# Kernel tuning notes

Hardware: AMD Instinct MI355X
Metric: run time of the kernel (lower is better)

The kernel has to match this reference:

```python
import jax, jax.numpy as jnp
import numpy as np

N = 10000          # nodes
E = 320000         # edges (~32 neighbors/node)
HID = 128          # hidden_channels
NF = 128           # num_filters
NG = 50            # num_gaussians
NB = 6             # num_interactions
CUT = 10.0         # cutoff


def ssp(x):
    # ShiftedSoftplus: softplus(x) - log(2)
    return jax.nn.softplus(x) - jnp.log(2.0).astype(x.dtype)


def setup_inputs() -> dict:
    key = jax.random.key(0)
    ks = jax.random.split(key, 16)
    z = jax.random.randint(ks[0], (N,), 0, 100)
    pos = jax.random.uniform(ks[1], (N, 3), dtype=jnp.float32) * 5.0  # box so d < cutoff
    row = jax.random.randint(ks[2], (E,), 0, N)
    off = jax.random.randint(ks[3], (E,), 1, N)  # avoid self-loops (radius_graph excludes them)
    col = (row + off) % N
    edge_index = jnp.stack([row, col], axis=0)
    nrm = lambda k, s: 0.1 * jax.random.normal(k, s, dtype=jnp.float32)
    return {
        "z": z,
        "pos": pos,
        "edge_index": edge_index,
        "emb": nrm(ks[4], (100, HID)),
        "mlp_w1": nrm(ks[5], (NB, NG, NF)),
        "mlp_b1": jnp.zeros((NB, NF), jnp.float32),
        "mlp_w2": nrm(ks[6], (NB, NF, NF)),
        "mlp_b2": jnp.zeros((NB, NF), jnp.float32),
        "cl1_w": nrm(ks[7], (NB, HID, NF)),
        "cl2_w": nrm(ks[8], (NB, NF, HID)),
        "cl2_b": jnp.zeros((NB, HID), jnp.float32),
        "lin_w": nrm(ks[9], (NB, HID, HID)),
        "lin_b": jnp.zeros((NB, HID), jnp.float32),
        "out_w1": nrm(ks[10], (HID, HID // 2)),
        "out_b1": jnp.zeros((HID // 2,), jnp.float32),
        "out_w2": nrm(ks[11], (HID // 2, 1)),
        "out_b2": jnp.zeros((1,), jnp.float32),
    }


def schnet_fwd(z, pos, edge_index, emb, mlp_w1, mlp_b1, mlp_w2, mlp_b2,
               cl1_w, cl2_w, cl2_b, lin_w, lin_b, out_w1, out_b1, out_w2, out_b2):
    row, col = edge_index[0], edge_index[1]  # j (source), i (target)
    d = jnp.linalg.norm(pos[row] - pos[col], axis=-1)  # [E]
    offsets = jnp.linspace(0.0, CUT, NG)
    coeff = -0.5 / (offsets[1] - offsets[0]) ** 2
    edge_attr = jnp.exp(coeff * (d[:, None] - offsets) ** 2)  # [E, NG]
    C = 0.5 * (jnp.cos(d * jnp.pi / CUT) + 1.0)  # cosine cutoff [E]
    h = emb[z]  # [N, HID]
    n = h.shape[0]
    for k in range(NB):
        # per-edge filter MLP
        W = ssp(edge_attr @ mlp_w1[k] + mlp_b1[k]) @ mlp_w2[k] + mlp_b2[k]
        W = W * C[:, None]  # [E, NF]
        x = h @ cl1_w[k]  # lin1 (no bias) [N, NF]
        msg = x[row] * W  # gather + modulate
        agg = jax.ops.segment_sum(msg, col, num_segments=n)  # scatter-add to targets
        x = agg @ cl2_w[k] + cl2_b[k]  # lin2 [N, HID]
        x = ssp(x)
        x = x @ lin_w[k] + lin_b[k]  # InteractionBlock.lin
        h = h + x  # residual
    h = ssp(h @ out_w1 + out_b1)
    return h @ out_w2 + out_b2  # [N, 1]


def reference(z, pos, edge_index, emb, mlp_w1, mlp_b1, mlp_w2, mlp_b2,
              cl1_w, cl2_w, cl2_b, lin_w, lin_b, out_w1, out_b1, out_w2, out_b2):
    return schnet_fwd(z, pos, edge_index, emb, mlp_w1, mlp_b1, mlp_w2, mlp_b2,
                      cl1_w, cl2_w, cl2_b, lin_w, lin_b, out_w1, out_b1, out_w2, out_b2)
```

## Files before the change

### kernel.cpp

```cpp
#include <hip/hip_runtime.h>
#include <math.h>

#define N_NODES 10000
#define N_EDGES 320000
#define HID 128
#define NF 128
#define NG 50
#define NB 6
#define SCAN_CH 40
#define WFRAG_PER_K 24576
#define NWF_PER_MAT 32768
#define TBL_M 2048
#define DMAX 8.6602540378f

typedef __attribute__((ext_vector_type(8))) short bf16x8;
typedef __attribute__((ext_vector_type(4))) float f32x4;
typedef __attribute__((ext_vector_type(4))) unsigned int u32x4;

__device__ __forceinline__ int pi_map(int f) {
  return (f & ~31) | ((f & 15) << 1) | ((f >> 4) & 1);
}
__device__ __forceinline__ int pinv_map(int g) {
  return (g & ~31) | ((g & 1) << 4) | ((g & 31) >> 1);
}

__device__ __forceinline__ unsigned short f2bf(float f) {
  unsigned u = __float_as_uint(f);
  u += 0x7FFFu + ((u >> 16) & 1u);
  return (unsigned short)(u >> 16);
}
__device__ __forceinline__ float bf2f(unsigned short s) {
  return __uint_as_float(((unsigned)s) << 16);
}
__device__ __forceinline__ unsigned pack2f(float a, float b) {
  return ((__float_as_uint(a) + 0x8000u) >> 16) |
         ((__float_as_uint(b) + 0x8000u) & 0xFFFF0000u);
}
__device__ __forceinline__ float ssp_fast(float x) {
  float t = __expf(-fabsf(x));
  return fmaxf(x, 0.0f) + __logf(1.0f + t) - 0.69314718055994530942f;
}

__global__ __launch_bounds__(256) void k_embed(const int* __restrict__ z,
                                               const float* __restrict__ emb,
                                               float* __restrict__ h) {
  int t = blockIdx.x * 256 + threadIdx.x;
  if (t >= N_NODES * HID) return;
  int i = t >> 7, c = t & 127;
  h[t] = emb[z[i] * HID + c];
}

__global__ __launch_bounds__(256) void k_hist(const int* __restrict__ col,
                                              int* __restrict__ count) {
  int e = blockIdx.x * 256 + threadIdx.x;
  if (e < N_EDGES) atomicAdd(&count[col[e]], 1);
}

__global__ __launch_bounds__(256) void k_scan(const int* __restrict__ count,
                                              int* __restrict__ rowptr,
                                              int* __restrict__ cursor) {
  __shared__ int s_part[256];
  int t = threadIdx.x;
  int begin = t * SCAN_CH, end = min(begin + SCAN_CH, N_NODES);
  int s = 0;
  for (int i = begin; i < end; i++) s += count[i];
  s_part[t] = s;
  __syncthreads();
  for (int off = 1; off < 256; off <<= 1) {
    int v = (t >= off) ? s_part[t - off] : 0;
    __syncthreads();
    s_part[t] += v;
    __syncthreads();
  }
  int run = (t > 0) ? s_part[t - 1] : 0;
  for (int i = begin; i < end; i++) {
    rowptr[i] = run;
    cursor[i] = run;
    run += count[i];
  }
  if (t == 255) rowptr[N_NODES] = N_EDGES;
}

__global__ __launch_bounds__(256) void k_scatter(const int* __restrict__ row,
                                                 const int* __restrict__ col,
                                                 const float* __restrict__ pos,
                                                 int* __restrict__ cursor,
                                                 int2* __restrict__ sorted_ru) {
  int e = blockIdx.x * 256 + threadIdx.x;
  if (e >= N_EDGES) return;
  int c = col[e], r = row[e];
  float dx = pos[3 * r + 0] - pos[3 * c + 0];
  float dy = pos[3 * r + 1] - pos[3 * c + 1];
  float dz = pos[3 * r + 2] - pos[3 * c + 2];
  float d = sqrtf(dx * dx + dy * dy + dz * dz);
  int p = atomicAdd(&cursor[c], 1);
  float u = d * ((float)(TBL_M - 1) / DMAX);
  sorted_ru[p] = make_int2(r, __float_as_int(u));
}

__global__ __launch_bounds__(256) void k_pack(const float* __restrict__ w1,
                                              const float* __restrict__ w2,
                                              unsigned short* __restrict__ wf) {
  const float* w1k = w1 + (size_t)blockIdx.x * NG * NF;
  const float* w2k = w2 + (size_t)blockIdx.x * NF * NF;
  unsigned short* wfk = wf + (size_t)blockIdx.x * WFRAG_PER_K;
  for (int inst = threadIdx.x; inst < 3072; inst += 256) {
    int fi = inst >> 8;
    int wv = (inst >> 6) & 3;
    int lane = inst & 63;
    int r16 = lane & 15, kgrp = lane >> 4;
    bf16x8 v;
#pragma unroll
    for (int j = 0; j < 8; ++j) {
      float val;
      if (fi < 4) {
        int ncol = wv * 32 + r16 + (fi >> 1) * 16;
        int k = (fi & 1) * 32 + kgrp * 8 + j;
        val = (k < NG) ? w1k[k * NF + ncol] : 0.f;
      } else {
        int fi2 = fi - 4;
        int ncol = wv * 32 + r16 + (fi2 >> 2) * 16;
        int kpi = (fi2 & 3) * 32 + kgrp * 8 + j;
        val = w2k[pinv_map(kpi) * NF + ncol];
      }
      v[j] = (short)f2bf(val);
    }
    *(bf16x8*)&wfk[inst * 8] = v;
  }
}

__global__ __launch_bounds__(256) void k_packn(const float* __restrict__ cl1,
                                               const float* __restrict__ cl2,
                                               const float* __restrict__ lin,
                                               unsigned short* __restrict__ nwf) {
  const int mat = blockIdx.x;
  const float* src = (mat < 6) ? cl1 + (size_t)mat * HID * NF
                   : (mat < 12) ? cl2 + (size_t)(mat - 6) * NF * HID
                                : lin + (size_t)(mat - 12) * HID * HID;
  unsigned short* dst = nwf + (size_t)mat * NWF_PER_MAT;
  for (int inst = threadIdx.x; inst < 2048; inst += 256) {
    int fi = inst >> 8;
    int wv = (inst >> 6) & 3;
    int lane = inst & 63;
    int r16 = lane & 15, kgrp = lane >> 4;
    int ncol = wv * 32 + r16 + (fi >> 2) * 16;
    int kb = fi & 3;
    bf16x8 fh, fl;
#pragma unroll
    for (int j = 0; j < 8; ++j) {
      float val = src[(kb * 32 + kgrp * 8 + j) * 128 + ncol];
      unsigned short hh = f2bf(val);
      fh[j] = (short)hh;
      fl[j] = (short)f2bf(val - bf2f(hh));
    }
    *(bf16x8*)&dst[((fi * 4 + wv) * 64 + lane) * 8] = fh;
    *(bf16x8*)&dst[(((fi + 8) * 4 + wv) * 64 + lane) * 8] = fl;
  }
}

__device__ __forceinline__ void stage_hilo(unsigned short* s_hi, unsigned short* s_lo,
                                           int rr, int c4, float4 v) {
  int cs = c4 ^ ((rr & 7) << 3);
  unsigned hax = (__float_as_uint(v.x) + 0x8000u) & 0xFFFF0000u;
  unsigned hay = (__float_as_uint(v.y) + 0x8000u) & 0xFFFF0000u;
  unsigned haz = (__float_as_uint(v.z) + 0x8000u) & 0xFFFF0000u;
  unsigned haw = (__float_as_uint(v.w) + 0x8000u) & 0xFFFF0000u;
  float lx = v.x - __uint_as_float(hax);
  float ly = v.y - __uint_as_float(hay);
  float lz = v.z - __uint_as_float(haz);
  float lw = v.w - __uint_as_float(haw);
  *(uint2*)&s_hi[rr * 128 + cs] = make_uint2((hax >> 16) | hay, (haz >> 16) | haw);
  *(uint2*)&s_lo[rr * 128 + cs] = make_uint2(pack2f(lx, ly), pack2f(lz, lw));
}

__device__ __forceinline__ int swz_idx(int row, int col) {
  return row * 128 + (((col & ~7) ^ ((row & 7) << 3)) | (col & 7));
}

#define KSTEP(accA, accB, kb, BH_A, BL_A, BH_B, BL_B)                          \
  {                                                                            \
    bf16x8 ahi = *(const bf16x8*)&s_hi[r16 * 128 + (((kb) * 32 + kb0) ^ swz)]; \
    bf16x8 alo = *(const bf16x8*)&s_lo[r16 * 128 + (((kb) * 32 + kb0) ^ swz)]; \
    accA = __builtin_amdgcn_mfma_f32_16x16x32_bf16(ahi, BH_A, accA, 0, 0, 0);  \
    accA = __builtin_amdgcn_mfma_f32_16x16x32_bf16(alo, BH_A, accA, 0, 0, 0);  \
    accA = __builtin_amdgcn_mfma_f32_16x16x32_bf16(ahi, BL_A, accA, 0, 0, 0);  \
    accB = __builtin_amdgcn_mfma_f32_16x16x32_bf16(ahi, BH_B, accB, 0, 0, 0);  \
    accB = __builtin_amdgcn_mfma_f32_16x16x32_bf16(alo, BH_B, accB, 0, 0, 0);  \
    accB = __builtin_amdgcn_mfma_f32_16x16x32_bf16(ahi, BL_B, accB, 0, 0, 0);  \
  }
#define MFMA_HALF(A0, A1)                          \
  {                                                \
    KSTEP(A0, A1, 0, bh00, bl00, bh10, bl10);      \
    KSTEP(A0, A1, 1, bh01, bl01, bh11, bl11);      \
    KSTEP(A0, A1, 2, bh02, bl02, bh12, bl12);      \
    KSTEP(A0, A1, 3, bh03, bl03, bh13, bl13);      \
  }
#define LOAD_FRAGS(wfp)                                                              \
  const bf16x8* np = (const bf16x8*)(wfp);                                           \
  const bf16x8 bh00 = np[(0 * 4 + wvid) * 64 + lane], bh01 = np[(1 * 4 + wvid) * 64 + lane], \
               bh02 = np[(2 * 4 + wvid) * 64 + lane], bh03 = np[(3 * 4 + wvid) * 64 + lane], \
               bh10 = np[(4 * 4 + wvid) * 64 + lane], bh11 = np[(5 * 4 + wvid) * 64 + lane], \
               bh12 = np[(6 * 4 + wvid) * 64 + lane], bh13 = np[(7 * 4 + wvid) * 64 + lane], \
               bl00 = np[(8 * 4 + wvid) * 64 + lane], bl01 = np[(9 * 4 + wvid) * 64 + lane], \
               bl02 = np[(10 * 4 + wvid) * 64 + lane], bl03 = np[(11 * 4 + wvid) * 64 + lane], \
               bl10 = np[(12 * 4 + wvid) * 64 + lane], bl11 = np[(13 * 4 + wvid) * 64 + lane], \
               bl12 = np[(14 * 4 + wvid) * 64 + lane], bl13 = np[(15 * 4 + wvid) * 64 + lane];

__global__ __launch_bounds__(256) void k_ngemm(const float* __restrict__ in,
                                               const unsigned short* __restrict__ wf,
                                               unsigned* __restrict__ xb,
                                               int nrows) {
  __shared__ __align__(16) float s_buf[16 * 128];
  unsigned short* s_hi = (unsigned short*)s_buf;
  unsigned short* s_lo = s_hi + 16 * 128;
  float* s_out = s_buf;

  const int tid = threadIdx.x;
  const int lane = tid & 63;
  const int wvid = tid >> 6;
  const int r16 = lane & 15;
  const int kgrp = lane >> 4;
  const int kb0 = kgrp * 8;
  const int nc0 = wvid * 32 + r16;
  const int nc1 = nc0 + 16;
  const int r0 = blockIdx.x * 16;

#pragma unroll
  for (int j = 0; j < 2; ++j) {
    int idx4 = j * 256 + tid;
    int rr = idx4 >> 5;
    int c4 = (idx4 & 31) << 2;
    float4 v = make_float4(0.f, 0.f, 0.f, 0.f);
    if (r0 + rr < nrows) v = *(const float4*)&in[(size_t)(r0 + rr) * 128 + c4];
    stage_hilo(s_hi, s_lo, rr, c4, v);
  }
  LOAD_FRAGS(wf);
  __syncthreads();

  f32x4 a00 = {0.f, 0.f, 0.f, 0.f}, a01 = a00;
  const int swz = (r16 & 7) << 3;
  MFMA_HALF(a00, a01);
  __syncthreads();

#pragma unroll
  for (int r = 0; r < 4; ++r) {
    int er0 = kgrp * 4 + r;
    s_out[er0 * 128 + (nc0 ^ ((er0 & 7) << 2))] = a00[r];
    s_out[er0 * 128 + (nc1 ^ ((er0 & 7) << 2))] = a01[r];
  }
  __syncthreads();

#pragma unroll
  for (int j = 0; j < 2; ++j) {
    int idx4 = j * 256 + tid;
    int rr = idx4 >> 5;
    int c4 = (idx4 & 31) << 2;
    if (r0 + rr >= nrows) continue;
    int cs = c4 ^ ((rr & 7) << 2);
    float4 v = *(float4*)&s_out[rr * 128 + cs];
    uint2 pk = make_uint2(pack2f(v.x, v.y), pack2f(v.z, v.w));
    *(uint2*)&xb[(size_t)(r0 + rr) * 64 + (c4 >> 1)] = pk;
  }
}

__global__ __launch_bounds__(256) void k_ngemm2(const float* __restrict__ agg,
                                                const unsigned short* __restrict__ wf_cl2,
                                                const float* __restrict__ b_cl2,
                                                const unsigned short* __restrict__ wf_lin,
                                                const float* __restrict__ b_lin,
                                                float* __restrict__ h,
                                                int nrows) {
  __shared__ __align__(16) float s_buf[16 * 128];
  unsigned short* s_hi = (unsigned short*)s_buf;
  unsigned short* s_lo = s_hi + 16 * 128;
  float* s_out = s_buf;

  const int tid = threadIdx.x;
  const int lane = tid & 63;
  const int wvid = tid >> 6;
  const int r16 = lane & 15;
  const int kgrp = lane >> 4;
  const int kb0 = kgrp * 8;
  const int nc0 = wvid * 32 + r16;
  const int nc1 = nc0 + 16;
  const int r0 = blockIdx.x * 16;
  const int swz = (r16 & 7) << 3;

#pragma unroll
  for (int j = 0; j < 2; ++j) {
    int idx4 = j * 256 + tid;
    int rr = idx4 >> 5;
    int c4 = (idx4 & 31) << 2;
    float4 v = make_float4(0.f, 0.f, 0.f, 0.f);
    if (r0 + rr < nrows) v = *(const float4*)&agg[(size_t)(r0 + rr) * 128 + c4];
    stage_hilo(s_hi, s_lo, rr, c4, v);
  }
  const float bc0 = b_cl2[nc0], bc1 = b_cl2[nc1];
  const float bl0_ = b_lin[nc0], bl1_ = b_lin[nc1];
  __syncthreads();

  f32x4 a00 = {0.f, 0.f, 0.f, 0.f}, a01 = a00;
  {
    LOAD_FRAGS(wf_cl2);
    MFMA_HALF(a00, a01);
  }
  __syncthreads();

#pragma unroll
  for (int r = 0; r < 4; ++r) {
    int er0 = kgrp * 4 + r;
    float t00 = ssp_fast(a00[r] + bc0);
    float t01 = ssp_fast(a01[r] + bc1);
    unsigned u;
    u = (__float_as_uint(t00) + 0x8000u) & 0xFFFF0000u;
    s_hi[swz_idx(er0, nc0)] = (unsigned short)(u >> 16);
    s_lo[swz_idx(er0, nc0)] = (unsigned short)(pack2f(t00 - __uint_as_float(u), 0.f));
    u = (__float_as_uint(t01) + 0x8000u) & 0xFFFF0000u;
    s_hi[swz_idx(er0, nc1)] = (unsigned short)(u >> 16);
    s_lo[swz_idx(er0, nc1)] = (unsigned short)(pack2f(t01 - __uint_as_float(u), 0.f));
  }
  __syncthreads();

  f32x4 c00 = {0.f, 0.f, 0.f, 0.f}, c01 = c00;
  {
    LOAD_FRAGS(wf_lin);
    MFMA_HALF(c00, c01);
  }
  __syncthreads();

#pragma unroll
  for (int r = 0; r < 4; ++r) {
    int er0 = kgrp * 4 + r;
    s_out[er0 * 128 + (nc0 ^ ((er0 & 7) << 2))] = c00[r] + bl0_;
    s_out[er0 * 128 + (nc1 ^ ((er0 & 7) << 2))] = c01[r] + bl1_;
  }
  __syncthreads();

#pragma unroll
  for (int j = 0; j < 2; ++j) {
    int idx4 = j * 256 + tid;
    int rr = idx4 >> 5;
    int c4 = (idx4 & 31) << 2;
    if (r0 + rr >= nrows) continue;
    int cs = c4 ^ ((rr & 7) << 2);
    float4 v = *(float4*)&s_out[rr * 128 + cs];
    float* dst = &h[(size_t)(r0 + rr) * 128 + c4];
    float4 o = *(const float4*)dst;
    v.x += o.x; v.y += o.y; v.z += o.z; v.w += o.w;
    *(float4*)dst = v;
  }
}

__global__ __launch_bounds__(256) void k_ngemm3(const float* __restrict__ agg,
                                                const unsigned short* __restrict__ wf_cl2,
                                                const float* __restrict__ b_cl2,
                                                const unsigned short* __restrict__ wf_lin,
                                                const float* __restrict__ b_lin,
                                                const unsigned short* __restrict__ wf_cl1n,
                                                float* __restrict__ h,
                                                unsigned* __restrict__ xb,
                                                int nrows) {
  __shared__ __align__(16) float s_buf[16 * 128];
  unsigned short* s_hi = (unsigned short*)s_buf;
  unsigned short* s_lo = s_hi + 16 * 128;
  float* s_out = s_buf;

  const int tid = threadIdx.x;
  const int lane = tid & 63;
  const int wvid = tid >> 6;
  const int r16 = lane & 15;
  const int kgrp = lane >> 4;
  const int kb0 = kgrp * 8;
  const int nc0 = wvid * 32 + r16;
  const int nc1 = nc0 + 16;
  const int r0 = blockIdx.x * 16;
  const int swz = (r16 & 7) << 3;

#pragma unroll
  for (int j = 0; j < 2; ++j) {
    int idx4 = j * 256 + tid;
    int rr = idx4 >> 5;
    int c4 = (idx4 & 31) << 2;
    float4 v = make_float4(0.f, 0.f, 0.f, 0.f);
    if (r0 + rr < nrows) v = *(const float4*)&agg[(size_t)(r0 + rr) * 128 + c4];
    stage_hilo(s_hi, s_lo, rr, c4, v);
  }
  const float bc0 = b_cl2[nc0], bc1 = b_cl2[nc1];
  const float bl0_ = b_lin[nc0], bl1_ = b_lin[nc1];
  __syncthreads();

  f32x4 a00 = {0.f, 0.f, 0.f, 0.f}, a01 = a00;
  {
    LOAD_FRAGS(wf_cl2);
    MFMA_HALF(a00, a01);
  }
  __syncthreads();

#pragma unroll
  for (int r = 0; r < 4; ++r) {
    int er0 = kgrp * 4 + r;
    float t00 = ssp_fast(a00[r] + bc0);
    float t01 = ssp_fast(a01[r] + bc1);
    unsigned u;
    u = (__float_as_uint(t00) + 0x8000u) & 0xFFFF0000u;
    s_hi[swz_idx(er0, nc0)] = (unsigned short)(u >> 16);
    s_lo[swz_idx(er0, nc0)] = (unsigned short)(pack2f(t00 - __uint_as_float(u), 0.f));
    u = (__float_as_uint(t01) + 0x8000u) & 0xFFFF0000u;
    s_hi[swz_idx(er0, nc1)] = (unsigned short)(u >> 16);
    s_lo[swz_idx(er0, nc1)] = (unsigned short)(pack2f(t01 - __uint_as_float(u), 0.f));
  }
  __syncthreads();

  f32x4 c00 = {0.f, 0.f, 0.f, 0.f}, c01 = c00;
  {
    LOAD_FRAGS(wf_lin);
    MFMA_HALF(c00, c01);
  }
  __syncthreads();

#pragma unroll
  for (int r = 0; r < 4; ++r) {
    int er0 = kgrp * 4 + r;
    s_out[er0 * 128 + (nc0 ^ ((er0 & 7) << 2))] = c00[r] + bl0_;
    s_out[er0 * 128 + (nc1 ^ ((er0 & 7) << 2))] = c01[r] + bl1_;
  }
  __syncthreads();

  float4 vv[2];
#pragma unroll
  for (int j = 0; j < 2; ++j) {
    int idx4 = j * 256 + tid;
    int rr = idx4 >> 5;
    int c4 = (idx4 & 31) << 2;
    int cs = c4 ^ ((rr & 7) << 2);
    float4 v = *(float4*)&s_out[rr * 128 + cs];
    if (r0 + rr < nrows) {
      float4 o = *(const float4*)&h[(size_t)(r0 + rr) * 128 + c4];
      v.x += o.x; v.y += o.y; v.z += o.z; v.w += o.w;
    } else {
      v = make_float4(0.f, 0.f, 0.f, 0.f);
    }
    vv[j] = v;
  }
  __syncthreads();
#pragma unroll
  for (int j = 0; j < 2; ++j) {
    int idx4 = j * 256 + tid;
    int rr = idx4 >> 5;
    int c4 = (idx4 & 31) << 2;
    stage_hilo(s_hi, s_lo, rr, c4, vv[j]);
    if (r0 + rr < nrows) *(float4*)&h[(size_t)(r0 + rr) * 128 + c4] = vv[j];
  }
  __syncthreads();

  a00 = (f32x4){0.f, 0.f, 0.f, 0.f}; a01 = a00;
  {
    LOAD_FRAGS(wf_cl1n);
    MFMA_HALF(a00, a01);
  }
  __syncthreads();

#pragma unroll
  for (int r = 0; r < 4; ++r) {
    int er0 = kgrp * 4 + r;
    s_out[er0 * 128 + (nc0 ^ ((er0 & 7) << 2))] = a00[r];
    s_out[er0 * 128 + (nc1 ^ ((er0 & 7) << 2))] = a01[r];
  }
  __syncthreads();

#pragma unroll
  for (int j = 0; j < 2; ++j) {
    int idx4 = j * 256 + tid;
    int rr = idx4 >> 5;
    int c4 = (idx4 & 31) << 2;
    if (r0 + rr >= nrows) continue;
    int cs = c4 ^ ((rr & 7) << 2);
    float4 v = *(float4*)&s_out[rr * 128 + cs];
    uint2 pk = make_uint2(pack2f(v.x, v.y), pack2f(v.z, v.w));
    *(uint2*)&xb[(size_t)(r0 + rr) * 64 + (c4 >> 1)] = pk;
  }
}

__global__ __launch_bounds__(256) void k_tbuild(
    const unsigned short* __restrict__ wf_all, const float* __restrict__ b1_all,
    const float* __restrict__ b2_all, float* __restrict__ T_all) {
  __shared__ __align__(16) unsigned short s_rbf[128 * 64];
  __shared__ __align__(16) unsigned short s_t1[128 * 128];
  __shared__ float s_C[128];

  const int kk = blockIdx.x >> 4;
  const int sb = blockIdx.x & 15;
  const int s0 = sb * 128;
  const unsigned short* wf = wf_all + (size_t)kk * WFRAG_PER_K;
  const float* b1 = b1_all + (size_t)kk * NF;
  const float* b2 = b2_all + (size_t)kk * NF;
  float* T = T_all + (size_t)kk * TBL_M * NF;

  const int tid = threadIdx.x;
  const int lane = tid & 63;
  const int wvid = tid >> 6;
  const int r16 = lane & 15;
  const int kgrp = lane >> 4;
  const int kb0 = kgrp * 8;
  const int nc0 = wvid * 32 + r16;
  const int nc1 = nc0 + 16;
  const int pcol = wvid * 32 + 2 * r16;

  const bf16x8* wp = (const bf16x8*)wf;
#define FR(fi) wp[((fi) * 4 + wvid) * 64 + lane]
  const bf16x8 w1_00 = FR(0), w1_10 = FR(1), w1_01 = FR(2), w1_11 = FR(3);
  const bf16x8 w2_00 = FR(4), w2_10 = FR(5), w2_20 = FR(6), w2_30 = FR(7);
  const bf16x8 w2_01 = FR(8), w2_11 = FR(9), w2_21 = FR(10), w2_31 = FR(11);
#undef FR
  const float b1n0 = b1[nc0], b1n1 = b1[nc1];
  const float b2n0 = b2[nc0], b2n1 = b2[nc1];

  {
    const int e = tid >> 1, gh = tid & 1;
    const float d = (float)(s0 + e) * (DMAX / (float)(TBL_M - 1));
    if (gh == 0) s_C[e] = 0.5f * (__cosf(d * 0.31415926535897932f) + 1.0f);
    const float step = 10.0f / 49.0f;
    const float coeff = -0.5f / (step * step);
    const int swz = (e & 7) << 3;
#pragma unroll
    for (int o = 0; o < 4; ++o) {
      int g0 = gh * 32 + o * 8;
      float vv[8];
#pragma unroll
      for (int j = 0; j < 8; ++j) {
        int g = g0 + j;
        float t = d - step * (float)g;
        vv[j] = (g < NG) ? __expf(coeff * t * t) : 0.0f;
      }
      u32x4 pk;
      pk[0] = pack2f(vv[0], vv[1]);
      pk[1] = pack2f(vv[2], vv[3]);
      pk[2] = pack2f(vv[4], vv[5]);
      pk[3] = pack2f(vv[6], vv[7]);
      *(u32x4*)&s_rbf[e * 64 + (g0 ^ swz)] = pk;
    }
  }
  __syncthreads();

  {
    const int swz = (r16 & 7) << 3;
    for (int mt = 0; mt < 8; ++mt) {
      const unsigned short* rp = &s_rbf[(mt * 16 + r16) * 64];
      bf16x8 a0 = *(const bf16x8*)&rp[(0 + kb0) ^ swz];
      bf16x8 a1 = *(const bf16x8*)&rp[(32 + kb0) ^ swz];
      f32x4 ac0 = {0.f, 0.f, 0.f, 0.f};
      f32x4 ac1 = {0.f, 0.f, 0.f, 0.f};
      ac0 = __builtin_amdgcn_mfma_f32_16x16x32_bf16(a0, w1_00, ac0, 0, 0, 0);
      ac0 = __builtin_amdgcn_mfma_f32_16x16x32_bf16(a1, w1_10, ac0, 0, 0, 0);
      ac1 = __builtin_amdgcn_mfma_f32_16x16x32_bf16(a0, w1_01, ac1, 0, 0, 0);
      ac1 = __builtin_amdgcn_mfma_f32_16x16x32_bf16(a1, w1_11, ac1, 0, 0, 0);
#pragma unroll
      for (int r = 0; r < 4; ++r) {
        int er = mt * 16 + kgrp * 4 + r;
        float v0 = ssp_fast(ac0[r] + b1n0);
        float v1 = ssp_fast(ac1[r] + b1n1);
        *(unsigned*)&s_t1[er * 128 + (pcol ^ ((er & 7) << 3))] = pack2f(v0, v1);
      }
    }
  }
  __syncthreads();

  {
    const int swz = (r16 & 7) << 3;
    for (int mt = 0; mt < 8; ++mt) {
      const unsigned short* tp = &s_t1[(mt * 16 + r16) * 128];
      bf16x8 a0 = *(const bf16x8*)&tp[(0 + kb0) ^ swz];
      bf16x8 a1 = *(const bf16x8*)&tp[(32 + kb0) ^ swz];
      bf16x8 a2 = *(const bf16x8*)&tp[(64 + kb0) ^ swz];
      bf16x8 a3 = *(const bf16x8*)&tp[(96 + kb0) ^ swz];
      f32x4 ac0 = {0.f, 0.f, 0.f, 0.f};
      f32x4 ac1 = {0.f, 0.f, 0.f, 0.f};
      ac0 = __builtin_amdgcn_mfma_f32_16x16x32_bf16(a0, w2_00, ac0, 0, 0, 0);
      ac0 = __builtin_amdgcn_mfma_f32_16x16x32_bf16(a1, w2_10, ac0, 0, 0, 0);
      ac0 = __builtin_amdgcn_mfma_f32_16x16x32_bf16(a2, w2_20, ac0, 0, 0, 0);
      ac0 = __builtin_amdgcn_mfma_f32_16x16x32_bf16(a3, w2_30, ac0, 0, 0, 0);
      ac1 = __builtin_amdgcn_mfma_f32_16x16x32_bf16(a0, w2_01, ac1, 0, 0, 0);
      ac1 = __builtin_amdgcn_mfma_f32_16x16x32_bf16(a1, w2_11, ac1, 0, 0, 0);
      ac1 = __builtin_amdgcn_mfma_f32_16x16x32_bf16(a2, w2_21, ac1, 0, 0, 0);
      ac1 = __builtin_amdgcn_mfma_f32_16x16x32_bf16(a3, w2_31, ac1, 0, 0, 0);
#pragma unroll
      for (int r = 0; r < 4; ++r) {
        int er = mt * 16 + kgrp * 4 + r;
        float Cc = s_C[er];
        float2 v = make_float2((ac0[r] + b2n0) * Cc, (ac1[r] + b2n1) * Cc);
        *(float2*)&T[(size_t)(s0 + er) * NF + pcol] = v;
      }
    }
  }
}

__global__ __launch_bounds__(256) void k_tpack(const float* __restrict__ T_all,
                                               unsigned* __restrict__ Tp_all) {
  size_t t = (size_t)blockIdx.x * 256 + threadIdx.x;
  int f = (int)(t & 127);
  size_t rem = t >> 7;
  int i = (int)(rem & (TBL_M - 1));
  int kk = (int)(rem >> 11);
  const float* T = T_all + (size_t)kk * TBL_M * NF;
  int pf = pi_map(f);
  float lo = T[(size_t)i * NF + pf];
  float hi = T[(size_t)min(i + 1, TBL_M - 1) * NF + pf];
  Tp_all[t] = pack2f(lo, hi);
}

__global__ __launch_bounds__(256) void k_aggr(const int2* __restrict__ ru,
                                              const int* __restrict__ rowptr,
                                              const unsigned* __restrict__ Tp,
                                              const unsigned* __restrict__ xb,
                                              float* __restrict__ agg) {
  __shared__ int2 s_ru[256];
  __shared__ float s_part[3 * 128];
  const int tid = threadIdx.x;
  const int wvid = tid >> 6;
  const int lane = tid & 63;
  const int sub = lane >> 5;
  const int l32 = lane & 31;
  const int f4 = l32 * 4;
  const int n = blockIdx.x;
  const int beg = rowptr[n], end = rowptr[n + 1];

  float a0 = 0.f, a1 = 0.f, a2 = 0.f, a3 = 0.f;
  for (int cs = beg; cs < end; cs += 256) {
    const int cnt = min(256, end - cs);
    if (tid < cnt) s_ru[tid] = ru[cs + tid];
    __syncthreads();
#define EDGE(J)                                                                  \
    {                                                                            \
      int j_ = (J);                                                              \
      bool valid_ = j_ < cnt;                                                    \
      int2 p_ = s_ru[valid_ ? j_ : 0];                                           \
      float u_ = __int_as_float(p_.y);                                           \
      int i0_ = min((int)u_, TBL_M - 2);                                         \
      float fr_ = u_ - (float)i0_;                                               \
      u32x4 t_ = *(const u32x4*)&Tp[(size_t)i0_ * NF + f4];                      \
      uint2 xw_ = *(const uint2*)&xb[(size_t)p_.x * 64 + l32 * 2];               \
      float vm_ = valid_ ? 1.0f : 0.0f;                                          \
      float lo_, hi_, w_;                                                        \
      lo_ = __uint_as_float(t_[0] << 16); hi_ = __uint_as_float(t_[0] & 0xFFFF0000u); \
      w_ = fmaf(fr_, hi_ - lo_, lo_) * vm_;                                      \
      a0 = fmaf(w_, __uint_as_float(xw_.x << 16), a0);                           \
      lo_ = __uint_as_float(t_[1] << 16); hi_ = __uint_as_float(t_[1] & 0xFFFF0000u); \
      w_ = fmaf(fr_, hi_ - lo_, lo_) * vm_;                                      \
      a1 = fmaf(w_, __uint_as_float(xw_.x & 0xFFFF0000u), a1);                   \
      lo_ = __uint_as_float(t_[2] << 16); hi_ = __uint_as_float(t_[2] & 0xFFFF0000u); \
      w_ = fmaf(fr_, hi_ - lo_, lo_) * vm_;                                      \
      a2 = fmaf(w_, __uint_as_float(xw_.y << 16), a2);                           \
      lo_ = __uint_as_float(t_[3] << 16); hi_ = __uint_as_float(t_[3] & 0xFFFF0000u); \
      w_ = fmaf(fr_, hi_ - lo_, lo_) * vm_;                                      \
      a3 = fmaf(w_, __uint_as_float(xw_.y & 0xFFFF0000u), a3);                   \
    }
    for (int jb = 0; jb < cnt; jb += 16) {
      EDGE(jb + wvid * 2 + sub);
      EDGE(jb + 8 + wvid * 2 + sub);
    }
#undef EDGE
    __syncthreads();
  }

  a0 += __shfl_xor(a0, 32);
  a1 += __shfl_xor(a1, 32);
  a2 += __shfl_xor(a2, 32);
  a3 += __shfl_xor(a3, 32);

  if (wvid > 0 && sub == 0) {
    *(float4*)&s_part[(wvid - 1) * 128 + f4] = make_float4(a0, a1, a2, a3);
  }
  __syncthreads();
  if (wvid == 0 && sub == 0) {
#pragma unroll
    for (int w = 0; w < 3; ++w) {
      float4 v = *(float4*)&s_part[w * 128 + f4];
      a0 += v.x; a1 += v.y; a2 += v.z; a3 += v.w;
    }
    *(float4*)&agg[(size_t)n * NF + f4] = make_float4(a0, a1, a2, a3);
  }
}

__global__ __launch_bounds__(256) void k_out(const float* __restrict__ h,
                                             const float* __restrict__ w1,
                                             const float* __restrict__ b1,
                                             const float* __restrict__ w2,
                                             const float* __restrict__ b2,
                                             float* __restrict__ out) {
  int wid = threadIdx.x >> 6;
  int lane = threadIdx.x & 63;
  int i = blockIdx.x * 4 + wid;
  if (i >= N_NODES) return;
  const float* __restrict__ hr = h + i * HID;
  float acc = b1[lane];
#pragma unroll 8
  for (int k = 0; k < HID; k++) acc = fmaf(hr[k], w1[k * 64 + lane], acc);
  float p = ssp_fast(acc) * w2[lane];
#pragma unroll
  for (int off = 32; off; off >>= 1) p += __shfl_down(p, off);
  if (lane == 0) out[i] = p + b2[0];
}

extern "C" void kernel_launch(void* const* d_in, const int* in_sizes, int n_in,
                              void* d_out, int out_size, void* d_ws, size_t ws_size,
                              hipStream_t stream) {
  const int* z = (const int*)d_in[0];
  const float* pos = (const float*)d_in[1];
  const int* eidx = (const int*)d_in[2];
  const float* emb = (const float*)d_in[3];
  const float* mlp_w1 = (const float*)d_in[4];
  const float* mlp_b1 = (const float*)d_in[5];
  const float* mlp_w2 = (const float*)d_in[6];
  const float* mlp_b2 = (const float*)d_in[7];
  const float* cl1_w = (const float*)d_in[8];
  const float* cl2_w = (const float*)d_in[9];
  const float* cl2_b = (const float*)d_in[10];
  const float* lin_w = (const float*)d_in[11];
  const float* lin_b = (const float*)d_in[12];
  const float* out_w1 = (const float*)d_in[13];
  const float* out_b1 = (const float*)d_in[14];
  const float* out_w2 = (const float*)d_in[15];
  const float* out_b2 = (const float*)d_in[16];
  float* out = (float*)d_out;

  float* h = (float*)d_ws;
  float* agg = h + N_NODES * HID;
  unsigned* xb = (unsigned*)(agg + N_NODES * HID);
  int* count = (int*)(xb + N_NODES * 64);
  int* rowptr = count + 10240;
  int* cursor = rowptr + 10240;
  int2* sorted_ru = (int2*)(cursor + 10240);
  unsigned short* wfrag = (unsigned short*)(sorted_ru + N_EDGES);
  unsigned short* nwf = wfrag + (size_t)NB * WFRAG_PER_K;
  float* Tbl = (float*)(nwf + (size_t)18 * NWF_PER_MAT);
  unsigned* Tp = (unsigned*)(Tbl + (size_t)NB * TBL_M * NF);
  const int* row = eidx;
  const int* col = eidx + N_EDGES;

  hipMemsetAsync(count, 0, 10240 * sizeof(int), stream);
  k_hist<<<(N_EDGES + 255) / 256, 256, 0, stream>>>(col, count);
  k_scan<<<1, 256, 0, stream>>>(count, rowptr, cursor);
  k_scatter<<<(N_EDGES + 255) / 256, 256, 0, stream>>>(row, col, pos, cursor,
                                                       sorted_ru);

  k_pack<<<NB, 256, 0, stream>>>(mlp_w1, mlp_w2, wfrag);
  k_packn<<<18, 256, 0, stream>>>(cl1_w, cl2_w, lin_w, nwf);
  k_tbuild<<<NB * 16, 256, 0, stream>>>(wfrag, mlp_b1, mlp_b2, Tbl);
  k_tpack<<<(NB * TBL_M * NF) / 256, 256, 0, stream>>>(Tbl, Tp);

  k_embed<<<(N_NODES * HID + 255) / 256, 256, 0, stream>>>(z, emb, h);

  const int NGB = (N_NODES + 15) / 16;
  k_ngemm<<<NGB, 256, 0, stream>>>(h, nwf + (size_t)0 * NWF_PER_MAT, xb, N_NODES);
  for (int k = 0; k < NB; k++) {
    k_aggr<<<N_NODES, 256, 0, stream>>>(sorted_ru, rowptr,
                                        Tp + (size_t)k * TBL_M * NF, xb, agg);
    if (k < NB - 1) {
      k_ngemm3<<<NGB, 256, 0, stream>>>(
          agg, nwf + (size_t)(6 + k) * NWF_PER_MAT, cl2_b + (size_t)k * HID,
          nwf + (size_t)(12 + k) * NWF_PER_MAT, lin_b + (size_t)k * HID,
          nwf + (size_t)(k + 1) * NWF_PER_MAT, h, xb, N_NODES);
    } else {
      k_ngemm2<<<NGB, 256, 0, stream>>>(
          agg, nwf + (size_t)(6 + k) * NWF_PER_MAT, cl2_b + (size_t)k * HID,
          nwf + (size_t)(12 + k) * NWF_PER_MAT, lin_b + (size_t)k * HID, h, N_NODES);
    }
  }

  k_out<<<(N_NODES + 3) / 4, 256, 0, stream>>>(h, out_w1, out_b1, out_w2, out_b2, out);
}
```

Baseline: 316.3 us.

## Fuse edge aggregation into node GEMM kernel with double-buffered xb

Merges the per-node edge aggregation into the interaction-block node GEMM kernel, so each 16-node block gathers its incoming edges into shared memory and then runs the cl2, lin and next cl1 GEMMs. This removes the agg round-trip through global memory and one launch per layer. The xb buffer is double-buffered so one layer can read the old features while the next are written. In exchange, aggregation parallelism drops from one 256-thread block per node to 16 nodes per block, with half-wave loops over edges and no cross-wave reduction. This may hurt latency hiding and load balance on the gather.

```diff
diff --git a/kernel.cpp b/kernel.cpp
--- a/kernel.cpp
+++ b/kernel.cpp
@@ -240,224 +240,6 @@
   f32x4 a00 = {0.f, 0.f, 0.f, 0.f}, a01 = a00;
   const int swz = (r16 & 7) << 3;
   MFMA_HALF(a00, a01);
-  __syncthreads();
-
-#pragma unroll
-  for (int r = 0; r < 4; ++r) {
-    int er0 = kgrp * 4 + r;
-    s_out[er0 * 128 + (nc0 ^ ((er0 & 7) << 2))] = a00[r];
-    s_out[er0 * 128 + (nc1 ^ ((er0 & 7) << 2))] = a01[r];
-  }
-  __syncthreads();
-
-#pragma unroll
-  for (int j = 0; j < 2; ++j) {
-    int idx4 = j * 256 + tid;
-    int rr = idx4 >> 5;
-    int c4 = (idx4 & 31) << 2;
-    if (r0 + rr >= nrows) continue;
-    int cs = c4 ^ ((rr & 7) << 2);
-    float4 v = *(float4*)&s_out[rr * 128 + cs];
-    uint2 pk = make_uint2(pack2f(v.x, v.y), pack2f(v.z, v.w));
-    *(uint2*)&xb[(size_t)(r0 + rr) * 64 + (c4 >> 1)] = pk;
-  }
-}
-
-__global__ __launch_bounds__(256) void k_ngemm2(const float* __restrict__ agg,
-                                                const unsigned short* __restrict__ wf_cl2,
-                                                const float* __restrict__ b_cl2,
-                                                const unsigned short* __restrict__ wf_lin,
-                                                const float* __restrict__ b_lin,
-                                                float* __restrict__ h,
-                                                int nrows) {
-  __shared__ __align__(16) float s_buf[16 * 128];
-  unsigned short* s_hi = (unsigned short*)s_buf;
-  unsigned short* s_lo = s_hi + 16 * 128;
-  float* s_out = s_buf;
-
-  const int tid = threadIdx.x;
-  const int lane = tid & 63;
-  const int wvid = tid >> 6;
-  const int r16 = lane & 15;
-  const int kgrp = lane >> 4;
-  const int kb0 = kgrp * 8;
-  const int nc0 = wvid * 32 + r16;
-  const int nc1 = nc0 + 16;
-  const int r0 = blockIdx.x * 16;
-  const int swz = (r16 & 7) << 3;
-
-#pragma unroll
-  for (int j = 0; j < 2; ++j) {
-    int idx4 = j * 256 + tid;
-    int rr = idx4 >> 5;
-    int c4 = (idx4 & 31) << 2;
-    float4 v = make_float4(0.f, 0.f, 0.f, 0.f);
-    if (r0 + rr < nrows) v = *(const float4*)&agg[(size_t)(r0 + rr) * 128 + c4];
-    stage_hilo(s_hi, s_lo, rr, c4, v);
-  }
-  const float bc0 = b_cl2[nc0], bc1 = b_cl2[nc1];
-  const float bl0_ = b_lin[nc0], bl1_ = b_lin[nc1];
-  __syncthreads();
-
-  f32x4 a00 = {0.f, 0.f, 0.f, 0.f}, a01 = a00;
-  {
-    LOAD_FRAGS(wf_cl2);
-    MFMA_HALF(a00, a01);
-  }
-  __syncthreads();
-
-#pragma unroll
-  for (int r = 0; r < 4; ++r) {
-    int er0 = kgrp * 4 + r;
-    float t00 = ssp_fast(a00[r] + bc0);
-    float t01 = ssp_fast(a01[r] + bc1);
-    unsigned u;
-    u = (__float_as_uint(t00) + 0x8000u) & 0xFFFF0000u;
-    s_hi[swz_idx(er0, nc0)] = (unsigned short)(u >> 16);
-    s_lo[swz_idx(er0, nc0)] = (unsigned short)(pack2f(t00 - __uint_as_float(u), 0.f));
-    u = (__float_as_uint(t01) + 0x8000u) & 0xFFFF0000u;
-    s_hi[swz_idx(er0, nc1)] = (unsigned short)(u >> 16);
-    s_lo[swz_idx(er0, nc1)] = (unsigned short)(pack2f(t01 - __uint_as_float(u), 0.f));
-  }
-  __syncthreads();
-
-  f32x4 c00 = {0.f, 0.f, 0.f, 0.f}, c01 = c00;
-  {
-    LOAD_FRAGS(wf_lin);
-    MFMA_HALF(c00, c01);
-  }
-  __syncthreads();
-
-#pragma unroll
-  for (int r = 0; r < 4; ++r) {
-    int er0 = kgrp * 4 + r;
-    s_out[er0 * 128 + (nc0 ^ ((er0 & 7) << 2))] = c00[r] + bl0_;
-    s_out[er0 * 128 + (nc1 ^ ((er0 & 7) << 2))] = c01[r] + bl1_;
-  }
-  __syncthreads();
-
-#pragma unroll
-  for (int j = 0; j < 2; ++j) {
-    int idx4 = j * 256 + tid;
-    int rr = idx4 >> 5;
-    int c4 = (idx4 & 31) << 2;
-    if (r0 + rr >= nrows) continue;
-    int cs = c4 ^ ((rr & 7) << 2);
-    float4 v = *(float4*)&s_out[rr * 128 + cs];
-    float* dst = &h[(size_t)(r0 + rr) * 128 + c4];
-    float4 o = *(const float4*)dst;
-    v.x += o.x; v.y += o.y; v.z += o.z; v.w += o.w;
-    *(float4*)dst = v;
-  }
-}
-
-__global__ __launch_bounds__(256) void k_ngemm3(const float* __restrict__ agg,
-                                                const unsigned short* __restrict__ wf_cl2,
-                                                const float* __restrict__ b_cl2,
-                                                const unsigned short* __restrict__ wf_lin,
-                                                const float* __restrict__ b_lin,
-                                                const unsigned short* __restrict__ wf_cl1n,
-                                                float* __restrict__ h,
-                                                unsigned* __restrict__ xb,
-                                                int nrows) {
-  __shared__ __align__(16) float s_buf[16 * 128];
-  unsigned short* s_hi = (unsigned short*)s_buf;
-  unsigned short* s_lo = s_hi + 16 * 128;
-  float* s_out = s_buf;
-
-  const int tid = threadIdx.x;
-  const int lane = tid & 63;
-  const int wvid = tid >> 6;
-  const int r16 = lane & 15;
-  const int kgrp = lane >> 4;
-  const int kb0 = kgrp * 8;
-  const int nc0 = wvid * 32 + r16;
-  const int nc1 = nc0 + 16;
-  const int r0 = blockIdx.x * 16;
-  const int swz = (r16 & 7) << 3;
-
-#pragma unroll
-  for (int j = 0; j < 2; ++j) {
-    int idx4 = j * 256 + tid;
-    int rr = idx4 >> 5;
-    int c4 = (idx4 & 31) << 2;
-    float4 v = make_float4(0.f, 0.f, 0.f, 0.f);
-    if (r0 + rr < nrows) v = *(const float4*)&agg[(size_t)(r0 + rr) * 128 + c4];
-    stage_hilo(s_hi, s_lo, rr, c4, v);
-  }
-  const float bc0 = b_cl2[nc0], bc1 = b_cl2[nc1];
-  const float bl0_ = b_lin[nc0], bl1_ = b_lin[nc1];
-  __syncthreads();
-
-  f32x4 a00 = {0.f, 0.f, 0.f, 0.f}, a01 = a00;
-  {
-    LOAD_FRAGS(wf_cl2);
-    MFMA_HALF(a00, a01);
-  }
-  __syncthreads();
-
-#pragma unroll
-  for (int r = 0; r < 4; ++r) {
-    int er0 = kgrp * 4 + r;
-    float t00 = ssp_fast(a00[r] + bc0);
-    float t01 = ssp_fast(a01[r] + bc1);
-    unsigned u;
-    u = (__float_as_uint(t00) + 0x8000u) & 0xFFFF0000u;
-    s_hi[swz_idx(er0, nc0)] = (unsigned short)(u >> 16);
-    s_lo[swz_idx(er0, nc0)] = (unsigned short)(pack2f(t00 - __uint_as_float(u), 0.f));
-    u = (__float_as_uint(t01) + 0x8000u) & 0xFFFF0000u;
-    s_hi[swz_idx(er0, nc1)] = (unsigned short)(u >> 16);
-    s_lo[swz_idx(er0, nc1)] = (unsigned short)(pack2f(t01 - __uint_as_float(u), 0.f));
-  }
-  __syncthreads();
-
-  f32x4 c00 = {0.f, 0.f, 0.f, 0.f}, c01 = c00;
-  {
-    LOAD_FRAGS(wf_lin);
-    MFMA_HALF(c00, c01);
-  }
-  __syncthreads();
-
-#pragma unroll
-  for (int r = 0; r < 4; ++r) {
-    int er0 = kgrp * 4 + r;
-    s_out[er0 * 128 + (nc0 ^ ((er0 & 7) << 2))] = c00[r] + bl0_;
-    s_out[er0 * 128 + (nc1 ^ ((er0 & 7) << 2))] = c01[r] + bl1_;
-  }
-  __syncthreads();
-
-  float4 vv[2];
-#pragma unroll
-  for (int j = 0; j < 2; ++j) {
-    int idx4 = j * 256 + tid;
-    int rr = idx4 >> 5;
-    int c4 = (idx4 & 31) << 2;
-    int cs = c4 ^ ((rr & 7) << 2);
-    float4 v = *(float4*)&s_out[rr * 128 + cs];
-    if (r0 + rr < nrows) {
-      float4 o = *(const float4*)&h[(size_t)(r0 + rr) * 128 + c4];
-      v.x += o.x; v.y += o.y; v.z += o.z; v.w += o.w;
-    } else {
-      v = make_float4(0.f, 0.f, 0.f, 0.f);
-    }
-    vv[j] = v;
-  }
-  __syncthreads();
-#pragma unroll
-  for (int j = 0; j < 2; ++j) {
-    int idx4 = j * 256 + tid;
-    int rr = idx4 >> 5;
-    int c4 = (idx4 & 31) << 2;
-    stage_hilo(s_hi, s_lo, rr, c4, vv[j]);
-    if (r0 + rr < nrows) *(float4*)&h[(size_t)(r0 + rr) * 128 + c4] = vv[j];
-  }
-  __syncthreads();
-
-  a00 = (f32x4){0.f, 0.f, 0.f, 0.f}; a01 = a00;
-  {
-    LOAD_FRAGS(wf_cl1n);
-    MFMA_HALF(a00, a01);
-  }
   __syncthreads();
 
 #pragma unroll
@@ -608,76 +390,198 @@
   Tp_all[t] = pack2f(lo, hi);
 }
 
-__global__ __launch_bounds__(256) void k_aggr(const int2* __restrict__ ru,
-                                              const int* __restrict__ rowptr,
-                                              const unsigned* __restrict__ Tp,
-                                              const unsigned* __restrict__ xb,
-                                              float* __restrict__ agg) {
-  __shared__ int2 s_ru[256];
-  __shared__ float s_part[3 * 128];
+#define LERP_ACC(t_, fr_, xw_)                                                   \
+  {                                                                              \
+    float lo_, hi_, w_;                                                          \
+    lo_ = __uint_as_float(t_[0] << 16); hi_ = __uint_as_float(t_[0] & 0xFFFF0000u); \
+    w_ = fmaf(fr_, hi_ - lo_, lo_);                                              \
+    a0 = fmaf(w_, __uint_as_float(xw_.x << 16), a0);                             \
+    lo_ = __uint_as_float(t_[1] << 16); hi_ = __uint_as_float(t_[1] & 0xFFFF0000u); \
+    w_ = fmaf(fr_, hi_ - lo_, lo_);                                              \
+    a1 = fmaf(w_, __uint_as_float(xw_.x & 0xFFFF0000u), a1);                     \
+    lo_ = __uint_as_float(t_[2] << 16); hi_ = __uint_as_float(t_[2] & 0xFFFF0000u); \
+    w_ = fmaf(fr_, hi_ - lo_, lo_);                                              \
+    a2 = fmaf(w_, __uint_as_float(xw_.y << 16), a2);                             \
+    lo_ = __uint_as_float(t_[3] << 16); hi_ = __uint_as_float(t_[3] & 0xFFFF0000u); \
+    w_ = fmaf(fr_, hi_ - lo_, lo_);                                              \
+    a3 = fmaf(w_, __uint_as_float(xw_.y & 0xFFFF0000u), a3);                     \
+  }
+
+template <bool LAST>
+__global__ __launch_bounds__(256) void k_fuse(
+    const int2* __restrict__ ru, const int* __restrict__ rowptr,
+    const unsigned* __restrict__ Tp, const unsigned* __restrict__ xb_in,
+    const unsigned short* __restrict__ wf_cl2, const float* __restrict__ b_cl2,
+    const unsigned short* __restrict__ wf_lin, const float* __restrict__ b_lin,
+    const unsigned short* __restrict__ wf_cl1n,
+    float* __restrict__ h, unsigned* __restrict__ xb_out, int nrows) {
+  __shared__ __align__(16) float s_agg[16 * 128];
+  __shared__ __align__(16) float s_buf[16 * 128];
+  unsigned short* s_hi = (unsigned short*)s_buf;
+  unsigned short* s_lo = s_hi + 16 * 128;
+  float* s_out = s_buf;
+
   const int tid = threadIdx.x;
+  const int lane = tid & 63;
   const int wvid = tid >> 6;
-  const int lane = tid & 63;
-  const int sub = lane >> 5;
-  const int l32 = lane & 31;
-  const int f4 = l32 * 4;
-  const int n = blockIdx.x;
-  const int beg = rowptr[n], end = rowptr[n + 1];
-
-  float a0 = 0.f, a1 = 0.f, a2 = 0.f, a3 = 0.f;
-  for (int cs = beg; cs < end; cs += 256) {
-    const int cnt = min(256, end - cs);
-    if (tid < cnt) s_ru[tid] = ru[cs + tid];
-    __syncthreads();
-#define EDGE(J)                                                                  \
-    {                                                                            \
-      int j_ = (J);                                                              \
-      bool valid_ = j_ < cnt;                                                    \
-      int2 p_ = s_ru[valid_ ? j_ : 0];                                           \
-      float u_ = __int_as_float(p_.y);                                           \
-      int i0_ = min((int)u_, TBL_M - 2);                                         \
-      float fr_ = u_ - (float)i0_;                                               \
-      u32x4 t_ = *(const u32x4*)&Tp[(size_t)i0_ * NF + f4];                      \
-      uint2 xw_ = *(const uint2*)&xb[(size_t)p_.x * 64 + l32 * 2];               \
-      float vm_ = valid_ ? 1.0f : 0.0f;                                          \
-      float lo_, hi_, w_;                                                        \
-      lo_ = __uint_as_float(t_[0] << 16); hi_ = __uint_as_float(t_[0] & 0xFFFF0000u); \
-      w_ = fmaf(fr_, hi_ - lo_, lo_) * vm_;                                      \
-      a0 = fmaf(w_, __uint_as_float(xw_.x << 16), a0);                           \
-      lo_ = __uint_as_float(t_[1] << 16); hi_ = __uint_as_float(t_[1] & 0xFFFF0000u); \
-      w_ = fmaf(fr_, hi_ - lo_, lo_) * vm_;                                      \
-      a1 = fmaf(w_, __uint_as_float(xw_.x & 0xFFFF0000u), a1);                   \
-      lo_ = __uint_as_float(t_[2] << 16); hi_ = __uint_as_float(t_[2] & 0xFFFF0000u); \
-      w_ = fmaf(fr_, hi_ - lo_, lo_) * vm_;                                      \
-      a2 = fmaf(w_, __uint_as_float(xw_.y << 16), a2);                           \
-      lo_ = __uint_as_float(t_[3] << 16); hi_ = __uint_as_float(t_[3] & 0xFFFF0000u); \
-      w_ = fmaf(fr_, hi_ - lo_, lo_) * vm_;                                      \
-      a3 = fmaf(w_, __uint_as_float(xw_.y & 0xFFFF0000u), a3);                   \
-    }
-    for (int jb = 0; jb < cnt; jb += 16) {
-      EDGE(jb + wvid * 2 + sub);
-      EDGE(jb + 8 + wvid * 2 + sub);
-    }
-#undef EDGE
-    __syncthreads();
-  }
-
-  a0 += __shfl_xor(a0, 32);
-  a1 += __shfl_xor(a1, 32);
-  a2 += __shfl_xor(a2, 32);
-  a3 += __shfl_xor(a3, 32);
-
-  if (wvid > 0 && sub == 0) {
-    *(float4*)&s_part[(wvid - 1) * 128 + f4] = make_float4(a0, a1, a2, a3);
-  }
-  __syncthreads();
-  if (wvid == 0 && sub == 0) {
-#pragma unroll
-    for (int w = 0; w < 3; ++w) {
-      float4 v = *(float4*)&s_part[w * 128 + f4];
-      a0 += v.x; a1 += v.y; a2 += v.z; a3 += v.w;
-    }
-    *(float4*)&agg[(size_t)n * NF + f4] = make_float4(a0, a1, a2, a3);
+  const int r16 = lane & 15;
+  const int kgrp = lane >> 4;
+  const int kb0 = kgrp * 8;
+  const int nc0 = wvid * 32 + r16;
+  const int nc1 = nc0 + 16;
+  const int r0 = blockIdx.x * 16;
+  const int swz = (r16 & 7) << 3;
+
+  {
+    const int hw = tid >> 5;
+    const int l32 = tid & 31;
+    const int f4 = l32 * 4;
+    for (int nn = hw; nn < 16; nn += 8) {
+      const int n = r0 + nn;
+      float a0 = 0.f, a1 = 0.f, a2 = 0.f, a3 = 0.f;
+      if (n < nrows) {
+        const int beg = rowptr[n], end = rowptr[n + 1];
+        int e = beg;
+        for (; e + 2 <= end; e += 2) {
+          int2 pA = ru[e], pB = ru[e + 1];
+          float uA = __int_as_float(pA.y);
+          int iA = min((int)uA, TBL_M - 2);
+          float frA = uA - (float)iA;
+          u32x4 tA = *(const u32x4*)&Tp[(size_t)iA * NF + f4];
+          uint2 xA = *(const uint2*)&xb_in[(size_t)pA.x * 64 + l32 * 2];
+          float uB = __int_as_float(pB.y);
+          int iB = min((int)uB, TBL_M - 2);
+          float frB = uB - (float)iB;
+          u32x4 tB = *(const u32x4*)&Tp[(size_t)iB * NF + f4];
+          uint2 xB = *(const uint2*)&xb_in[(size_t)pB.x * 64 + l32 * 2];
+          LERP_ACC(tA, frA, xA);
+          LERP_ACC(tB, frB, xB);
+        }
+        if (e < end) {
+          int2 pA = ru[e];
+          float uA = __int_as_float(pA.y);
+          int iA = min((int)uA, TBL_M - 2);
+          float frA = uA - (float)iA;
+          u32x4 tA = *(const u32x4*)&Tp[(size_t)iA * NF + f4];
+          uint2 xA = *(const uint2*)&xb_in[(size_t)pA.x * 64 + l32 * 2];
+          LERP_ACC(tA, frA, xA);
+        }
+      }
+      *(float4*)&s_agg[nn * 128 + f4] = make_float4(a0, a1, a2, a3);
+    }
+  }
+  __syncthreads();
+
+#pragma unroll
+  for (int j = 0; j < 2; ++j) {
+    int idx4 = j * 256 + tid;
+    int rr = idx4 >> 5;
+    int c4 = (idx4 & 31) << 2;
+    stage_hilo(s_hi, s_lo, rr, c4, *(float4*)&s_agg[rr * 128 + c4]);
+  }
+  const float bc0 = b_cl2[nc0], bc1 = b_cl2[nc1];
+  const float bl0_ = b_lin[nc0], bl1_ = b_lin[nc1];
+  __syncthreads();
+
+  f32x4 a00 = {0.f, 0.f, 0.f, 0.f}, a01 = a00;
+  {
+    LOAD_FRAGS(wf_cl2);
+    MFMA_HALF(a00, a01);
+  }
+  __syncthreads();
+
+#pragma unroll
+  for (int r = 0; r < 4; ++r) {
+    int er0 = kgrp * 4 + r;
+    float t00 = ssp_fast(a00[r] + bc0);
+    float t01 = ssp_fast(a01[r] + bc1);
+    unsigned u;
+    u = (__float_as_uint(t00) + 0x8000u) & 0xFFFF0000u;
+    s_hi[swz_idx(er0, nc0)] = (unsigned short)(u >> 16);
+    s_lo[swz_idx(er0, nc0)] = (unsigned short)(pack2f(t00 - __uint_as_float(u), 0.f));
+    u = (__float_as_uint(t01) + 0x8000u) & 0xFFFF0000u;
+    s_hi[swz_idx(er0, nc1)] = (unsigned short)(u >> 16);
+    s_lo[swz_idx(er0, nc1)] = (unsigned short)(pack2f(t01 - __uint_as_float(u), 0.f));
+  }
+  __syncthreads();
+
+  f32x4 c00 = {0.f, 0.f, 0.f, 0.f}, c01 = c00;
+  {
+    LOAD_FRAGS(wf_lin);
+    MFMA_HALF(c00, c01);
+  }
+  __syncthreads();
+
+#pragma unroll
+  for (int r = 0; r < 4; ++r) {
+    int er0 = kgrp * 4 + r;
+    s_out[er0 * 128 + (nc0 ^ ((er0 & 7) << 2))] = c00[r] + bl0_;
+    s_out[er0 * 128 + (nc1 ^ ((er0 & 7) << 2))] = c01[r] + bl1_;
+  }
+  __syncthreads();
+
+  float4 vv[2];
+#pragma unroll
+  for (int j = 0; j < 2; ++j) {
+    int idx4 = j * 256 + tid;
+    int rr = idx4 >> 5;
+    int c4 = (idx4 & 31) << 2;
+    int cs = c4 ^ ((rr & 7) << 2);
+    float4 v = *(float4*)&s_out[rr * 128 + cs];
+    if (r0 + rr < nrows) {
+      float4 o = *(const float4*)&h[(size_t)(r0 + rr) * 128 + c4];
+      v.x += o.x; v.y += o.y; v.z += o.z; v.w += o.w;
+    } else {
+      v = make_float4(0.f, 0.f, 0.f, 0.f);
+    }
+    vv[j] = v;
+  }
+  if (LAST) {
+#pragma unroll
+    for (int j = 0; j < 2; ++j) {
+      int idx4 = j * 256 + tid;
+      int rr = idx4 >> 5;
+      int c4 = (idx4 & 31) << 2;
+      if (r0 + rr < nrows) *(float4*)&h[(size_t)(r0 + rr) * 128 + c4] = vv[j];
+    }
+    return;
+  }
+  __syncthreads();
+#pragma unroll
+  for (int j = 0; j < 2; ++j) {
+    int idx4 = j * 256 + tid;
+    int rr = idx4 >> 5;
+    int c4 = (idx4 & 31) << 2;
+    stage_hilo(s_hi, s_lo, rr, c4, vv[j]);
+    if (r0 + rr < nrows) *(float4*)&h[(size_t)(r0 + rr) * 128 + c4] = vv[j];
+  }
+  __syncthreads();
+
+  a00 = (f32x4){0.f, 0.f, 0.f, 0.f}; a01 = a00;
+  {
+    LOAD_FRAGS(wf_cl1n);
+    MFMA_HALF(a00, a01);
+  }
+  __syncthreads();
+
+#pragma unroll
+  for (int r = 0; r < 4; ++r) {
+    int er0 = kgrp * 4 + r;
+    s_out[er0 * 128 + (nc0 ^ ((er0 & 7) << 2))] = a00[r];
+    s_out[er0 * 128 + (nc1 ^ ((er0 & 7) << 2))] = a01[r];
+  }
+  __syncthreads();
+
+#pragma unroll
+  for (int j = 0; j < 2; ++j) {
+    int idx4 = j * 256 + tid;
+    int rr = idx4 >> 5;
+    int c4 = (idx4 & 31) << 2;
+    if (r0 + rr >= nrows) continue;
+    int cs = c4 ^ ((rr & 7) << 2);
+    float4 v = *(float4*)&s_out[rr * 128 + cs];
+    uint2 pk = make_uint2(pack2f(v.x, v.y), pack2f(v.z, v.w));
+    *(uint2*)&xb_out[(size_t)(r0 + rr) * 64 + (c4 >> 1)] = pk;
   }
 }
 
@@ -724,9 +628,9 @@
   float* out = (float*)d_out;
 
   float* h = (float*)d_ws;
-  float* agg = h + N_NODES * HID;
-  unsigned* xb = (unsigned*)(agg + N_NODES * HID);
-  int* count = (int*)(xb + N_NODES * 64);
+  unsigned* xb0 = (unsigned*)(h + N_NODES * HID);
+  unsigned* xb1 = xb0 + N_NODES * 64;
+  int* count = (int*)(xb1 + N_NODES * 64);
   int* rowptr = count + 10240;
   int* cursor = rowptr + 10240;
   int2* sorted_ru = (int2*)(cursor + 10240);
@@ -751,19 +655,24 @@
   k_embed<<<(N_NODES * HID + 255) / 256, 256, 0, stream>>>(z, emb, h);
 
   const int NGB = (N_NODES + 15) / 16;
-  k_ngemm<<<NGB, 256, 0, stream>>>(h, nwf + (size_t)0 * NWF_PER_MAT, xb, N_NODES);
+  k_ngemm<<<NGB, 256, 0, stream>>>(h, nwf + (size_t)0 * NWF_PER_MAT, xb0, N_NODES);
+
+  unsigned* xbufs[2] = {xb0, xb1};
   for (int k = 0; k < NB; k++) {
-    k_aggr<<<N_NODES, 256, 0, stream>>>(sorted_ru, rowptr,
-                                        Tp + (size_t)k * TBL_M * NF, xb, agg);
+    unsigned* xin = xbufs[k & 1];
+    unsigned* xout = xbufs[(k + 1) & 1];
     if (k < NB - 1) {
-      k_ngemm3<<<NGB, 256, 0, stream>>>(
-          agg, nwf + (size_t)(6 + k) * NWF_PER_MAT, cl2_b + (size_t)k * HID,
+      k_fuse<false><<<NGB, 256, 0, stream>>>(
+          sorted_ru, rowptr, Tp + (size_t)k * TBL_M * NF, xin,
+          nwf + (size_t)(6 + k) * NWF_PER_MAT, cl2_b + (size_t)k * HID,
           nwf + (size_t)(12 + k) * NWF_PER_MAT, lin_b + (size_t)k * HID,
-          nwf + (size_t)(k + 1) * NWF_PER_MAT, h, xb, N_NODES);
+          nwf + (size_t)(k + 1) * NWF_PER_MAT, h, xout, N_NODES);
     } else {
-      k_ngemm2<<<NGB, 256, 0, stream>>>(
-          agg, nwf + (size_t)(6 + k) * NWF_PER_MAT, cl2_b + (size_t)k * HID,
-          nwf + (size_t)(12 + k) * NWF_PER_MAT, lin_b + (size_t)k * HID, h, N_NODES);
+      k_fuse<true><<<NGB, 256, 0, stream>>>(
+          sorted_ru, rowptr, Tp + (size_t)k * TBL_M * NF, xin,
+          nwf + (size_t)(6 + k) * NWF_PER_MAT, cl2_b + (size_t)k * HID,
+          nwf + (size_t)(12 + k) * NWF_PER_MAT, lin_b + (size_t)k * HID,
+          nwf, h, xout, N_NODES);
     }
   }
 
```

After: 350.4 us. 1.11x slower.
